# Kernel optimization log

Measured on AMD Instinct MI355X. Metric: run time of the kernel, lower is better.

The kernel has to match this reference:

```python
import jax, jax.numpy as jnp
import numpy as np

B_, S, I, H = 16, 2048, 256, 512


def setup_inputs() -> dict:
    key = jax.random.key(0)
    k0, k1, k2, k3, k4 = jax.random.split(key, 5)
    x = jax.random.normal(k0, (B_, S, I), dtype=jnp.float32)
    # stable LRU parameterization: lambda = exp(-exp(nu) + i*theta), |lambda| < 1
    nu = jax.random.uniform(k1, (H,), dtype=jnp.float32, minval=-3.0, maxval=0.0)
    theta = jax.random.uniform(k2, (H,), dtype=jnp.float32, minval=0.0, maxval=2.0 * np.pi)
    scale = np.float32(1.0 / np.sqrt(2 * I))
    B_re = jax.random.normal(k3, (H, I), dtype=jnp.float32) * scale
    B_im = jax.random.normal(k4, (H, I), dtype=jnp.float32) * scale
    return {"x": x, "nu": nu, "theta": theta, "B_re": B_re, "B_im": B_im}


def reference(x, nu, theta, B_re, B_im):
    # complex diagonal recurrence matrix, shape [H]
    lam = jnp.exp(-jnp.exp(nu) + 1j * theta).astype(jnp.complex64)
    # complex input projection Bx_t = (B_re + i B_im) @ x_t, shape [batch, seq, H]
    Bx = (jnp.einsum('bsi,hi->bsh', x, B_re)
          + 1j * jnp.einsum('bsi,hi->bsh', x, B_im)).astype(jnp.complex64)
    Bx_t = jnp.swapaxes(Bx, 0, 1)  # [seq, batch, H] for scan over time
    h0 = jnp.zeros((x.shape[0], lam.shape[0]), dtype=jnp.complex64)

    def step(h, bx):
        h = lam * h + bx  # h_t = lambda * h_{t-1} + B x_t
        return h, h

    _, outs = jax.lax.scan(step, h0, Bx_t)  # [seq, batch, H] complex
    outs = jnp.swapaxes(outs, 0, 1)  # [batch, seq, H]
    # concat_real_imag: [batch, seq, 2H] float32
    return jnp.concatenate([outs.real, outs.imag], axis=-1)
```

## Files before the change

kernel.cpp:

```cpp
#include <hip/hip_runtime.h>
#include <cstdint>
#include <cstddef>

#define BB 16
#define SS 2048
#define II 256
#define HH 512
#define MM (BB * SS)
#define NNC 1024
#define CHUNK 64
#define NCHUNK (SS / CHUNK)

using bf16x8 = __attribute__((ext_vector_type(8))) short;
using short8 = __attribute__((ext_vector_type(8))) short;
using f32x4  = __attribute__((ext_vector_type(4))) float;

typedef __attribute__((address_space(3))) uint32_t       lds_u32;
typedef __attribute__((address_space(1))) const uint32_t glb_u32;

__device__ __forceinline__ short f2bf(float f) {
    uint32_t u = __float_as_uint(f);
    u += 0x7fffu + ((u >> 16) & 1u);
    return (short)(u >> 16);
}
__device__ __forceinline__ uint32_t packf16(float a, float b) {
    union { _Float16 h[2]; uint32_t u; } cv;
    cv.h[0] = (_Float16)a; cv.h[1] = (_Float16)b;
    return cv.u;
}
__device__ __forceinline__ float2 unpackf16(uint32_t u) {
    union { uint32_t u; _Float16 h[2]; } cv; cv.u = u;
    return make_float2((float)cv.h[0], (float)cv.h[1]);
}

__global__ __launch_bounds__(256) void cvt_x(const float4* __restrict__ x,
                                             short8* __restrict__ xb) {
    int i = blockIdx.x * 256 + threadIdx.x;
    float4 v0 = x[2 * i], v1 = x[2 * i + 1];
    short8 o;
    o[0]=f2bf(v0.x); o[1]=f2bf(v0.y); o[2]=f2bf(v0.z); o[3]=f2bf(v0.w);
    o[4]=f2bf(v1.x); o[5]=f2bf(v1.y); o[6]=f2bf(v1.z); o[7]=f2bf(v1.w);
    xb[i] = o;
}

__global__ __launch_bounds__(256) void cvt_b(const float* __restrict__ Bre,
                                             const float* __restrict__ Bim,
                                             short* __restrict__ Bc) {
    int idx = blockIdx.x * 256 + threadIdx.x;
    int row = idx >> 5;
    int k0  = (idx & 31) << 3;
    const float* src = ((row & 1) ? Bim : Bre) + (size_t)(row >> 1) * II + k0;
    float4 v0 = *(const float4*)src;
    float4 v1 = *(const float4*)(src + 4);
    short8 o;
    o[0]=f2bf(v0.x); o[1]=f2bf(v0.y); o[2]=f2bf(v0.z); o[3]=f2bf(v0.w);
    o[4]=f2bf(v1.x); o[5]=f2bf(v1.y); o[6]=f2bf(v1.z); o[7]=f2bf(v1.w);
    *(short8*)(Bc + (size_t)row * II + k0) = o;
}

__global__ __launch_bounds__(256, 3) void gemm_pack(const short* __restrict__ Xb,
                                                    const short* __restrict__ Bc,
                                                    uint32_t* __restrict__ Y) {
    __shared__ short Al[2][128 * 32];
    __shared__ short Bl[2][128 * 32];

    const int mt = blockIdx.x >> 3;
    const int nt = blockIdx.x & 7;
    const int m0 = mt * 128, n0 = nt * 128;
    const int t  = threadIdx.x;
    const int w  = t >> 6, l = t & 63;
    const int fr = l & 15, fg = l >> 4;
    const int wr = w >> 1, wc = w & 1;

    f32x4 acc[4][4] = {};

#pragma unroll
    for (int i = 0; i < 2; ++i) {
        const int ch = i * 256 + t;
        __builtin_amdgcn_global_load_lds(
            (glb_u32*)(Xb + (size_t)(m0 + (ch >> 2)) * II + ((ch & 3) << 3)),
            (lds_u32*)&Al[0][ch * 8], 16, 0, 0);
        __builtin_amdgcn_global_load_lds(
            (glb_u32*)(Bc + (size_t)(n0 + (ch >> 2)) * II + ((ch & 3) << 3)),
            (lds_u32*)&Bl[0][ch * 8], 16, 0, 0);
    }
    __syncthreads();

    for (int ks = 0; ks < 8; ++ks) {
        const int cur = ks & 1, nxt = cur ^ 1;
        if (ks < 7) {
#pragma unroll
            for (int i = 0; i < 2; ++i) {
                const int ch = i * 256 + t;
                __builtin_amdgcn_global_load_lds(
                    (glb_u32*)(Xb + (size_t)(m0 + (ch >> 2)) * II + (ks + 1) * 32 + ((ch & 3) << 3)),
                    (lds_u32*)&Al[nxt][ch * 8], 16, 0, 0);
                __builtin_amdgcn_global_load_lds(
                    (glb_u32*)(Bc + (size_t)(n0 + (ch >> 2)) * II + (ks + 1) * 32 + ((ch & 3) << 3)),
                    (lds_u32*)&Bl[nxt][ch * 8], 16, 0, 0);
            }
        }
        bf16x8 a[4], b[4];
#pragma unroll
        for (int mi = 0; mi < 4; ++mi)
            a[mi] = *(const bf16x8*)&Al[cur][(wr * 64 + mi * 16 + fr) * 32 + fg * 8];
#pragma unroll
        for (int ni = 0; ni < 4; ++ni)
            b[ni] = *(const bf16x8*)&Bl[cur][(wc * 64 + ni * 16 + fr) * 32 + fg * 8];
#pragma unroll
        for (int mi = 0; mi < 4; ++mi)
#pragma unroll
            for (int ni = 0; ni < 4; ++ni)
                acc[mi][ni] = __builtin_amdgcn_mfma_f32_16x16x32_bf16(
                    a[mi], b[ni], acc[mi][ni], 0, 0, 0);
        __syncthreads();
    }

#pragma unroll
    for (int mi = 0; mi < 4; ++mi)
#pragma unroll
        for (int ni = 0; ni < 4; ++ni) {
            const int row0 = m0 + wr * 64 + mi * 16 + fg * 4;
            const int ncol = n0 + wc * 64 + ni * 16 + fr;
#pragma unroll
            for (int r = 0; r < 4; ++r) {
                float v = acc[mi][ni][r];
                float o = __shfl_xor(v, 1);
                if (!(fr & 1))
                    Y[(size_t)(row0 + r) * HH + (ncol >> 1)] = packf16(v, o);
            }
        }
}

__global__ __launch_bounds__(512) void scan_e(const uint32_t* __restrict__ Y,
                                              const float* __restrict__ nu,
                                              const float* __restrict__ th,
                                              float2* __restrict__ E) {
    const int g = blockIdx.x;
    const int b = g >> 5, c = g & 31;
    const int h = threadIdx.x;
    const float env = __expf(nu[h]);
    const float rad = __expf(-env);
    float s, cs; __sincosf(th[h], &s, &cs);
    const float lre = rad * cs, lim = rad * s;
    const uint32_t* base = Y + ((size_t)b * SS + (size_t)c * CHUNK) * HH + h;
    float hre = 0.f, him = 0.f;
#pragma unroll 8
    for (int t = 0; t < CHUNK; ++t) {
        float2 y = unpackf16(base[(size_t)t * HH]);
        const float nr = lre * hre - lim * him + y.x;
        him = lre * him + lim * hre + y.y;
        hre = nr;
    }
    E[(size_t)g * HH + h] = make_float2(hre, him);
}

__global__ __launch_bounds__(512) void carry(const float2* __restrict__ E,
                                             const float* __restrict__ nu,
                                             const float* __restrict__ th,
                                             float2* __restrict__ P) {
    const int b = blockIdx.x;
    const int h = threadIdx.x;
    const float env = __expf(nu[h]);
    const float rL  = __expf(-(float)CHUNK * env);
    float s, cs; __sincosf((float)CHUNK * th[h], &s, &cs);
    const float lre = rL * cs, lim = rL * s;
    float pre = 0.f, pim = 0.f;
#pragma unroll 4
    for (int c = 0; c < NCHUNK; ++c) {
        const size_t idx = ((size_t)b * NCHUNK + c) * HH + h;
        P[idx] = make_float2(pre, pim);
        const float2 e = E[idx];
        const float nr = lre * pre - lim * pim + e.x;
        pim = lre * pim + lim * pre + e.y;
        pre = nr;
    }
}

__global__ __launch_bounds__(512) void scan_final(const uint32_t* __restrict__ Y,
                                                  const float2* __restrict__ P,
                                                  const float* __restrict__ nu,
                                                  const float* __restrict__ th,
                                                  float* __restrict__ out) {
    const int g = blockIdx.x;
    const int b = g >> 5, c = g & 31;
    const int h = threadIdx.x;
    const float env = __expf(nu[h]);
    const float rad = __expf(-env);
    float s, cs; __sincosf(th[h], &s, &cs);
    const float lre = rad * cs, lim = rad * s;
    const float2 p = P[(size_t)g * HH + h];
    float hre = p.x, him = p.y;
    const uint32_t* yb = Y + ((size_t)b * SS + (size_t)c * CHUNK) * HH + h;
    float* ob = out + ((size_t)b * SS + (size_t)c * CHUNK) * NNC;
#pragma unroll 4
    for (int t = 0; t < CHUNK; ++t) {
        float2 y = unpackf16(yb[(size_t)t * HH]);
        const float nr = lre * hre - lim * him + y.x;
        him = lre * him + lim * hre + y.y;
        hre = nr;
        ob[(size_t)t * NNC + h]      = hre;
        ob[(size_t)t * NNC + HH + h] = him;
    }
}

extern "C" void kernel_launch(void* const* d_in, const int* in_sizes, int n_in,
                              void* d_out, int out_size, void* d_ws, size_t ws_size,
                              hipStream_t stream) {
    const float* x   = (const float*)d_in[0];
    const float* nu  = (const float*)d_in[1];
    const float* th  = (const float*)d_in[2];
    const float* Bre = (const float*)d_in[3];
    const float* Bim = (const float*)d_in[4];
    float* out = (float*)d_out;

    char* ws = (char*)d_ws;
    short*    Xb = (short*)ws;
    short*    Bc = (short*)(ws + (size_t)MM * II * 2);
    uint32_t* Y  = (uint32_t*)(ws + (size_t)MM * II * 2 + (size_t)NNC * II * 2);
    float2*   E  = (float2*)((char*)Y + (size_t)MM * HH * 4);
    float2*   P  = E + (size_t)BB * NCHUNK * HH;

    cvt_x<<<(MM * II / 8) / 256, 256, 0, stream>>>((const float4*)x, (short8*)Xb);
    cvt_b<<<(NNC * II / 8) / 256, 256, 0, stream>>>(Bre, Bim, Bc);
    gemm_pack<<<(MM / 128) * (NNC / 128), 256, 0, stream>>>(Xb, Bc, Y);
    scan_e<<<BB * NCHUNK, HH, 0, stream>>>(Y, nu, th, E);
    carry<<<BB, HH, 0, stream>>>(E, nu, th, P);
    scan_final<<<BB * NCHUNK, HH, 0, stream>>>(Y, P, nu, th, out);
}
```

Baseline: 101.0 us.

## Fuse chunk-end scan into GEMM epilogue and merge conversion kernels

The per-chunk end-state scan moves into the GEMM epilogue. Each block stages its packed fp16 tile in shared memory and 32 threads run the 64-step recurrence for each 16-channel group, writing chunk-end states straight to E. This removes the separate scan_e kernel, which had to re-read all of Y from global memory. The two bf16 conversion kernels are also merged into one launch. In exchange the GEMM epilogue gains four extra barriers and a short serial phase in which only 32 of 256 threads work, plus extra LDS that may reduce occupancy.

New measurement: 141.2 us. 1.4x slower.

```diff
diff --git a/kernel.cpp b/kernel.cpp
--- a/kernel.cpp
+++ b/kernel.cpp
@@ -8,8 +8,8 @@
 #define HH 512
 #define MM (BB * SS)
 #define NNC 1024
-#define CHUNK 64
-#define NCHUNK (SS / CHUNK)
+#define SCHUNK 64
+#define SNCHUNK 32
 
 using bf16x8 = __attribute__((ext_vector_type(8))) short;
 using short8 = __attribute__((ext_vector_type(8))) short;
@@ -33,36 +33,42 @@
     return make_float2((float)cv.h[0], (float)cv.h[1]);
 }
 
-__global__ __launch_bounds__(256) void cvt_x(const float4* __restrict__ x,
-                                             short8* __restrict__ xb) {
-    int i = blockIdx.x * 256 + threadIdx.x;
-    float4 v0 = x[2 * i], v1 = x[2 * i + 1];
-    short8 o;
-    o[0]=f2bf(v0.x); o[1]=f2bf(v0.y); o[2]=f2bf(v0.z); o[3]=f2bf(v0.w);
-    o[4]=f2bf(v1.x); o[5]=f2bf(v1.y); o[6]=f2bf(v1.z); o[7]=f2bf(v1.w);
-    xb[i] = o;
-}
-
-__global__ __launch_bounds__(256) void cvt_b(const float* __restrict__ Bre,
-                                             const float* __restrict__ Bim,
-                                             short* __restrict__ Bc) {
-    int idx = blockIdx.x * 256 + threadIdx.x;
-    int row = idx >> 5;
-    int k0  = (idx & 31) << 3;
-    const float* src = ((row & 1) ? Bim : Bre) + (size_t)(row >> 1) * II + k0;
-    float4 v0 = *(const float4*)src;
-    float4 v1 = *(const float4*)(src + 4);
-    short8 o;
-    o[0]=f2bf(v0.x); o[1]=f2bf(v0.y); o[2]=f2bf(v0.z); o[3]=f2bf(v0.w);
-    o[4]=f2bf(v1.x); o[5]=f2bf(v1.y); o[6]=f2bf(v1.z); o[7]=f2bf(v1.w);
-    *(short8*)(Bc + (size_t)row * II + k0) = o;
-}
-
-__global__ __launch_bounds__(256, 3) void gemm_pack(const short* __restrict__ Xb,
-                                                    const short* __restrict__ Bc,
-                                                    uint32_t* __restrict__ Y) {
-    __shared__ short Al[2][128 * 32];
-    __shared__ short Bl[2][128 * 32];
+__global__ __launch_bounds__(256) void cvt_xb(const float4* __restrict__ x,
+                                              short8* __restrict__ xb,
+                                              const float* __restrict__ Bre,
+                                              const float* __restrict__ Bim,
+                                              short* __restrict__ Bc) {
+    const int bid = blockIdx.x;
+    if (bid < 4096) {
+        int i = bid * 256 + threadIdx.x;
+        float4 v0 = x[2 * i], v1 = x[2 * i + 1];
+        short8 o;
+        o[0]=f2bf(v0.x); o[1]=f2bf(v0.y); o[2]=f2bf(v0.z); o[3]=f2bf(v0.w);
+        o[4]=f2bf(v1.x); o[5]=f2bf(v1.y); o[6]=f2bf(v1.z); o[7]=f2bf(v1.w);
+        xb[i] = o;
+    } else {
+        int idx = (bid - 4096) * 256 + threadIdx.x;
+        int row = idx >> 5;
+        int k0  = (idx & 31) << 3;
+        const float* src = ((row & 1) ? Bim : Bre) + (size_t)(row >> 1) * II + k0;
+        float4 v0 = *(const float4*)src;
+        float4 v1 = *(const float4*)(src + 4);
+        short8 o;
+        o[0]=f2bf(v0.x); o[1]=f2bf(v0.y); o[2]=f2bf(v0.z); o[3]=f2bf(v0.w);
+        o[4]=f2bf(v1.x); o[5]=f2bf(v1.y); o[6]=f2bf(v1.z); o[7]=f2bf(v1.w);
+        *(short8*)(Bc + (size_t)row * II + k0) = o;
+    }
+}
+
+__global__ __launch_bounds__(256, 3) void gemm_scanE(const short* __restrict__ Xb,
+                                                     const short* __restrict__ Bc,
+                                                     const float* __restrict__ nu,
+                                                     const float* __restrict__ th,
+                                                     uint32_t* __restrict__ Y,
+                                                     float2* __restrict__ E) {
+    __shared__ short    Al[2][128 * 32];
+    __shared__ short    Bl[2][128 * 32];
+    __shared__ uint32_t T2[128 * 17];
 
     const int mt = blockIdx.x >> 3;
     const int nt = blockIdx.x & 7;
@@ -130,29 +136,56 @@
                     Y[(size_t)(row0 + r) * HH + (ncol >> 1)] = packf16(v, o);
             }
         }
-}
-
-__global__ __launch_bounds__(512) void scan_e(const uint32_t* __restrict__ Y,
-                                              const float* __restrict__ nu,
-                                              const float* __restrict__ th,
-                                              float2* __restrict__ E) {
-    const int g = blockIdx.x;
-    const int b = g >> 5, c = g & 31;
-    const int h = threadIdx.x;
-    const float env = __expf(nu[h]);
-    const float rad = __expf(-env);
-    float s, cs; __sincosf(th[h], &s, &cs);
-    const float lre = rad * cs, lim = rad * s;
-    const uint32_t* base = Y + ((size_t)b * SS + (size_t)c * CHUNK) * HH + h;
-    float hre = 0.f, him = 0.f;
-#pragma unroll 8
-    for (int t = 0; t < CHUNK; ++t) {
-        float2 y = unpackf16(base[(size_t)t * HH]);
-        const float nr = lre * hre - lim * him + y.x;
-        him = lre * him + lim * hre + y.y;
-        hre = nr;
-    }
-    E[(size_t)g * HH + h] = make_float2(hre, him);
+
+    const int b_  = m0 >> 11;
+    const int c64 = (m0 >> 6) & 31;
+
+#pragma unroll
+    for (int p = 0; p < 4; ++p) {
+        if (wc == (p >> 1)) {
+#pragma unroll
+            for (int nn = 0; nn < 2; ++nn) {
+                const int ni = (p & 1) * 2 + nn;
+#pragma unroll
+                for (int mi = 0; mi < 4; ++mi)
+#pragma unroll
+                    for (int r = 0; r < 4; ++r) {
+                        const float v = acc[mi][ni][r];
+                        const float o = __shfl_xor(v, 1);
+                        if (!(fr & 1))
+                            T2[(wr * 64 + mi * 16 + fg * 4 + r) * 17 + nn * 8 + (fr >> 1)] =
+                                packf16(v, o);
+                    }
+            }
+        }
+        __syncthreads();
+
+        if (t < 32) {
+            const int chn = t & 15;
+            const int hc  = t >> 4;
+            const int gch = nt * 64 + p * 16 + chn;
+            const float env = __expf(nu[gch]);
+            const float rad = __expf(-env);
+            float s1, c1; __sincosf(th[gch], &s1, &c1);
+            const float lre = rad * c1, lim = rad * s1;
+            float hre = 0.f, him = 0.f;
+            for (int i0 = 0; i0 < 64; i0 += 8) {
+                uint32_t vv[8];
+#pragma unroll
+                for (int i = 0; i < 8; ++i)
+                    vv[i] = T2[(hc * 64 + i0 + i) * 17 + chn];
+#pragma unroll
+                for (int i = 0; i < 8; ++i) {
+                    const float2 v = unpackf16(vv[i]);
+                    const float nr = lre * hre - lim * him + v.x;
+                    him = lre * him + lim * hre + v.y;
+                    hre = nr;
+                }
+            }
+            E[((size_t)b_ * SNCHUNK + c64 + hc) * HH + gch] = make_float2(hre, him);
+        }
+        __syncthreads();
+    }
 }
 
 __global__ __launch_bounds__(512) void carry(const float2* __restrict__ E,
@@ -162,13 +195,13 @@
     const int b = blockIdx.x;
     const int h = threadIdx.x;
     const float env = __expf(nu[h]);
-    const float rL  = __expf(-(float)CHUNK * env);
-    float s, cs; __sincosf((float)CHUNK * th[h], &s, &cs);
+    const float rL  = __expf(-(float)SCHUNK * env);
+    float s, cs; __sincosf((float)SCHUNK * th[h], &s, &cs);
     const float lre = rL * cs, lim = rL * s;
     float pre = 0.f, pim = 0.f;
 #pragma unroll 4
-    for (int c = 0; c < NCHUNK; ++c) {
-        const size_t idx = ((size_t)b * NCHUNK + c) * HH + h;
+    for (int c = 0; c < SNCHUNK; ++c) {
+        const size_t idx = ((size_t)b * SNCHUNK + c) * HH + h;
         P[idx] = make_float2(pre, pim);
         const float2 e = E[idx];
         const float nr = lre * pre - lim * pim + e.x;
@@ -191,10 +224,10 @@
     const float lre = rad * cs, lim = rad * s;
     const float2 p = P[(size_t)g * HH + h];
     float hre = p.x, him = p.y;
-    const uint32_t* yb = Y + ((size_t)b * SS + (size_t)c * CHUNK) * HH + h;
-    float* ob = out + ((size_t)b * SS + (size_t)c * CHUNK) * NNC;
+    const uint32_t* yb = Y + ((size_t)b * SS + (size_t)c * SCHUNK) * HH + h;
+    float* ob = out + ((size_t)b * SS + (size_t)c * SCHUNK) * NNC;
 #pragma unroll 4
-    for (int t = 0; t < CHUNK; ++t) {
+    for (int t = 0; t < SCHUNK; ++t) {
         float2 y = unpackf16(yb[(size_t)t * HH]);
         const float nr = lre * hre - lim * him + y.x;
         him = lre * him + lim * hre + y.y;
@@ -219,12 +252,10 @@
     short*    Bc = (short*)(ws + (size_t)MM * II * 2);
     uint32_t* Y  = (uint32_t*)(ws + (size_t)MM * II * 2 + (size_t)NNC * II * 2);
     float2*   E  = (float2*)((char*)Y + (size_t)MM * HH * 4);
-    float2*   P  = E + (size_t)BB * NCHUNK * HH;
-
-    cvt_x<<<(MM * II / 8) / 256, 256, 0, stream>>>((const float4*)x, (short8*)Xb);
-    cvt_b<<<(NNC * II / 8) / 256, 256, 0, stream>>>(Bre, Bim, Bc);
-    gemm_pack<<<(MM / 128) * (NNC / 128), 256, 0, stream>>>(Xb, Bc, Y);
-    scan_e<<<BB * NCHUNK, HH, 0, stream>>>(Y, nu, th, E);
+    float2*   P  = E + (size_t)BB * SNCHUNK * HH;
+
+    cvt_xb<<<4096 + 128, 256, 0, stream>>>((const float4*)x, (short8*)Xb, Bre, Bim, Bc);
+    gemm_scanE<<<(MM / 128) * (NNC / 128), 256, 0, stream>>>(Xb, Bc, nu, th, Y, E);
     carry<<<BB, HH, 0, stream>>>(E, nu, th, P);
-    scan_final<<<BB * NCHUNK, HH, 0, stream>>>(Y, P, nu, th, out);
-}
+    scan_final<<<BB * SNCHUNK, HH, 0, stream>>>(Y, P, nu, th, out);
+}
```
